# Kernel tuning notes

Measured on AMD Instinct MI355X. Metric: run time of the kernel, lower is better.

Reference implementation:

```python
import jax, jax.numpy as jnp
import numpy as np

B, H, W, C, HEADS, SR = 4, 64, 64, 256, 8, 2
D = C // HEADS            # head dim = 32
SCALE = D ** -0.5
EPS = 1e-6


def _conv(x, w, stride, pad, groups):
    return jax.lax.conv_general_dilated(
        x, w, (stride, stride), [(pad, pad), (pad, pad)],
        feature_group_count=groups,
        dimension_numbers=('NCHW', 'OIHW', 'NCHW'))


def setup_inputs() -> dict:
    key = jax.random.key(0)
    ks = jax.random.split(key, 9)
    s = lambda fan: 1.0 / np.sqrt(fan)
    return {
        'x': jax.random.normal(ks[0], (B, H * W, C), jnp.float32),
        'dw_w': jax.random.normal(ks[1], (C, 1, 3, 3), jnp.float32) * s(9),
        'dw_b': jnp.zeros((C,), jnp.float32),
        'pw_w': jax.random.normal(ks[2], (C, C, 1, 1), jnp.float32) * s(C),
        'pw_b': jnp.zeros((C,), jnp.float32),
        'sr_w': jax.random.normal(ks[3], (C, 1, 3, 3), jnp.float32) * s(9),
        'ln_g': jnp.ones((C,), jnp.float32),
        'ln_b': jnp.zeros((C,), jnp.float32),
        'kv_w': jax.random.normal(ks[4], (2 * C, C), jnp.float32) * s(C),
        'kv_b': jnp.zeros((2 * C,), jnp.float32),
        'proj_w': jax.random.normal(ks[5], (C, C), jnp.float32) * s(C),
        'proj_b': jnp.zeros((C,), jnp.float32),
    }


def reference(x, dw_w, dw_b, pw_w, pw_b, sr_w, ln_g, ln_b, kv_w, kv_b, proj_w, proj_b):
    Bx, N, Cx = x.shape
    # Q path: depthwise-separable conv on the spatial layout
    xq = x.reshape(Bx, H, W, Cx).transpose(0, 3, 1, 2)          # (B,C,H,W)
    q = _conv(xq, dw_w, 1, 1, Cx) + dw_b[None, :, None, None]    # depthwise 3x3
    q = _conv(q, pw_w, 1, 0, 1) + pw_b[None, :, None, None]      # pointwise 1x1
    # 'b (h d) l w -> b h (l w) d'
    q = q.reshape(Bx, HEADS, D, H * W).transpose(0, 1, 3, 2)     # (B,h,N,d)

    # SR path for K/V: strided depthwise conv + LayerNorm
    x_ = _conv(xq, sr_w, SR, SR // 2, Cx)                        # (B,C,H/SR,W/SR)
    x_ = x_.reshape(Bx, Cx, -1).transpose(0, 2, 1)               # (B,M,C)
    mu = jnp.mean(x_, axis=-1, keepdims=True)
    var = jnp.mean(jnp.square(x_ - mu), axis=-1, keepdims=True)
    x_ = (x_ - mu) * jax.lax.rsqrt(var + EPS) * ln_g + ln_b

    kv = x_ @ kv_w.T + kv_b                                      # (B,M,2C)
    M = kv.shape[1]
    kv = kv.reshape(Bx, M, 2, HEADS, D).transpose(2, 0, 3, 1, 4) # (2,B,h,M,d)
    k, v = kv[0], kv[1]

    attn = jnp.einsum('bhnd,bhmd->bhnm', q, k) * SCALE           # (B,h,N,M)
    attn = jax.nn.softmax(attn, axis=-1)
    out = jnp.einsum('bhnm,bhmd->bhnd', attn, v)                 # (B,h,N,d)
    out = out.transpose(0, 2, 1, 3).reshape(Bx, N, Cx)           # (B,N,C)
    return out @ proj_w.T + proj_b
```

## Files before the change

### kernel.cpp

```cpp
#include <hip/hip_runtime.h>
#include <math.h>

#define BB 4
#define HH 64
#define WW 64
#define CC 256
#define NN 4096
#define MM 1024
#define LN_EPS 1e-6f
#define SLF (0.17677669529663687f * 1.4426950408889634f)

typedef __attribute__((ext_vector_type(8)))  short short8;
typedef __attribute__((ext_vector_type(16))) float f32x16;
typedef __attribute__((ext_vector_type(4)))  unsigned int uint32x4;

__device__ __forceinline__ ushort f2bf(float f) {
  unsigned u = __builtin_bit_cast(unsigned, f);
  u += 0x7fffu + ((u >> 16) & 1u);
  return (ushort)(u >> 16);
}
__device__ __forceinline__ float bf2f(ushort h) {
  unsigned u = ((unsigned)h) << 16;
  return __builtin_bit_cast(float, u);
}
#if __has_builtin(__builtin_amdgcn_exp2f)
#define EXP2F(x) __builtin_amdgcn_exp2f(x)
#else
#define EXP2F(x) exp2f(x)
#endif

__global__ __launch_bounds__(256) void pre_fused(
    const float* __restrict__ x, const float* __restrict__ dw_w,
    const float* __restrict__ dw_b, const float* __restrict__ sr_w,
    const float* __restrict__ ln_g, const float* __restrict__ ln_b,
    const float* __restrict__ pw_w, const float* __restrict__ kv_w,
    const float* __restrict__ proj_w,
    ushort* __restrict__ q1b, ushort* __restrict__ xsr,
    ushort* __restrict__ pwB, ushort* __restrict__ kvB,
    ushort* __restrict__ pjH, ushort* __restrict__ pjL) {
  int bid = blockIdx.x;
  int c = threadIdx.x;
  if (bid < 4096) {
    int b = bid >> 10, m = bid & 1023;
    int my = m >> 5, mx = m & 31;
    const float* xb = x + (size_t)b * NN * CC + c;
    float acc = 0.f;
#pragma unroll
    for (int dy = 0; dy < 3; ++dy) {
      int iy = 2 * my + dy - 1;
      if (iy < 0 || iy >= HH) continue;
#pragma unroll
      for (int dx = 0; dx < 3; ++dx) {
        int ix = 2 * mx + dx - 1;
        if (ix < 0 || ix >= WW) continue;
        acc += xb[(size_t)(iy * WW + ix) * CC] * sr_w[c * 9 + dy * 3 + dx];
      }
    }
    float v1 = acc, v2 = acc * acc;
#pragma unroll
    for (int s = 1; s < 64; s <<= 1) {
      v1 += __shfl_xor(v1, s);
      v2 += __shfl_xor(v2, s);
    }
    __shared__ float r1[4], r2[4];
    int lane = c & 63, wv = c >> 6;
    if (lane == 0) { r1[wv] = v1; r2[wv] = v2; }
    __syncthreads();
    float s1 = r1[0] + r1[1] + r1[2] + r1[3];
    float s2 = r2[0] + r2[1] + r2[2] + r2[3];
    float mu = s1 * (1.f / 256.f);
    float var = s2 * (1.f / 256.f) - mu * mu;
    float yv = (acc - mu) * rsqrtf(var + LN_EPS) * ln_g[c] + ln_b[c];
    xsr[((size_t)b * MM + m) * CC + c] = f2bf(yv);
  } else if (bid < 6144) {
    int id = bid - 4096;
    int b = id >> 9, r = id & 511;
    int y = r >> 3, seg = r & 7;
    int x0 = seg * 8;
    float wr[9];
#pragma unroll
    for (int i = 0; i < 9; ++i) wr[i] = dw_w[c * 9 + i];
    float bi = dw_b[c];
    const float* xb = x + (size_t)b * NN * CC + c;
    bool okT = (y > 0), okB = (y < 63);
    float a0, a1, a2, b0, b1, b2;
    if (x0 == 0) {
      a0 = a1 = a2 = 0.f;
    } else {
      a0 = okT ? xb[(size_t)((y - 1) * 64 + x0 - 1) * CC] : 0.f;
      a1 = xb[(size_t)(y * 64 + x0 - 1) * CC];
      a2 = okB ? xb[(size_t)((y + 1) * 64 + x0 - 1) * CC] : 0.f;
    }
    b0 = okT ? xb[(size_t)((y - 1) * 64 + x0) * CC] : 0.f;
    b1 = xb[(size_t)(y * 64 + x0) * CC];
    b2 = okB ? xb[(size_t)((y + 1) * 64 + x0) * CC] : 0.f;
    ushort* ob = q1b + ((size_t)b * NN + y * 64) * CC + c;
#pragma unroll 8
    for (int xx = x0; xx < x0 + 8; ++xx) {
      float c0v, c1v, c2v;
      if (xx < 63) {
        c0v = okT ? xb[(size_t)((y - 1) * 64 + xx + 1) * CC] : 0.f;
        c1v = xb[(size_t)(y * 64 + xx + 1) * CC];
        c2v = okB ? xb[(size_t)((y + 1) * 64 + xx + 1) * CC] : 0.f;
      } else {
        c0v = c1v = c2v = 0.f;
      }
      float acc = bi;
      acc += a0 * wr[0] + b0 * wr[1] + c0v * wr[2];
      acc += a1 * wr[3] + b1 * wr[4] + c1v * wr[5];
      acc += a2 * wr[6] + b2 * wr[7] + c2v * wr[8];
      ob[(size_t)xx * CC] = f2bf(acc);
      a0 = b0; a1 = b1; a2 = b2;
      b0 = c0v; b1 = c1v; b2 = c2v;
    }
  } else if (bid < 6208) {
    int i0 = (bid - 6144) * 1024 + c * 4;
    float4 v = *(const float4*)&pw_w[i0];
    ushort tmp[4] = {f2bf(v.x), f2bf(v.y), f2bf(v.z), f2bf(v.w)};
    *(uint2*)&pwB[i0] = *(uint2*)tmp;
  } else if (bid < 6336) {
    int i0 = (bid - 6208) * 1024 + c * 4;
    float4 v = *(const float4*)&kv_w[i0];
    ushort tmp[4] = {f2bf(v.x), f2bf(v.y), f2bf(v.z), f2bf(v.w)};
    *(uint2*)&kvB[i0] = *(uint2*)tmp;
  } else {
    int i0 = (bid - 6336) * 1024 + c * 4;
    float4 v = *(const float4*)&proj_w[i0];
    float vv[4] = {v.x, v.y, v.z, v.w};
    ushort th[4], tl[4];
#pragma unroll
    for (int j = 0; j < 4; ++j) {
      th[j] = f2bf(vv[j]);
      tl[j] = f2bf(vv[j] - bf2f(th[j]));
    }
    *(uint2*)&pjH[i0] = *(uint2*)th;
    *(uint2*)&pjL[i0] = *(uint2*)tl;
  }
}

__global__ __launch_bounds__(256) void gemm_qkv(
    const ushort* __restrict__ q1b, const ushort* __restrict__ xsr,
    const ushort* __restrict__ pwB, const float* __restrict__ pw_b,
    const ushort* __restrict__ kvB, const float* __restrict__ kv_b,
    ushort* __restrict__ qB, ushort* __restrict__ kB,
    ushort* __restrict__ vT) {
  __shared__ ushort smem[2][128 * 40];
  int bid = blockIdx.x;
  bool is0 = bid < 1024;
  const ushort* A;
  const ushort* W;
  const float* bias;
  int r0, c0;
  if (is0) {
    A = q1b; W = pwB; bias = pw_b;
    r0 = (bid >> 2) * 64; c0 = (bid & 3) * 64;
  } else {
    int sid = bid - 1024;
    A = xsr; W = kvB; bias = kv_b;
    r0 = (sid >> 3) * 64; c0 = (sid & 7) * 64;
  }
  const bool vmode = (!is0) && (c0 >= 256);

  int t = threadIdx.x;
  int lane = t & 63, w = t >> 6;
  int l31 = lane & 31, half = lane >> 5;
  int wr = w >> 1, wc = w & 1;
  int rowA = t >> 2, kq = (t & 3) * 8;

  f32x16 acc;
#pragma unroll
  for (int i = 0; i < 16; ++i) acc[i] = 0.f;

  short8 ra[2], rw[2];
  auto prefetch = [&](int kc, int s) {
    ra[s] = *(const short8*)&A[(size_t)(r0 + rowA) * 256 + kc + kq];
    rw[s] = *(const short8*)&W[(size_t)(c0 + rowA) * 256 + kc + kq];
  };
  auto store = [&](ushort* buf, int s) {
    *(short8*)&buf[rowA * 40 + kq] = ra[s];
    *(short8*)&buf[64 * 40 + rowA * 40 + kq] = rw[s];
  };

  prefetch(0, 0);
  store(smem[0], 0);
  prefetch(32, 1);
  __syncthreads();
#pragma unroll
  for (int i = 0; i < 8; ++i) {
    ushort* cur = smem[i & 1];
    ushort* nxt = smem[(i & 1) ^ 1];
    if (i < 7) store(nxt, (i + 1) & 1);
    if (i < 6) prefetch((i + 2) * 32, i & 1);
#pragma unroll
    for (int ks = 0; ks < 2; ++ks) {
      short8 af = *(const short8*)&cur[(wr * 32 + l31) * 40 + ks * 16 + half * 8];
      short8 wf = *(const short8*)&cur[64 * 40 + (wc * 32 + l31) * 40 + ks * 16 + half * 8];
      if (vmode)
        acc = __builtin_amdgcn_mfma_f32_32x32x16_bf16(wf, af, acc, 0, 0, 0);
      else
        acc = __builtin_amdgcn_mfma_f32_32x32x16_bf16(af, wf, acc, 0, 0, 0);
    }
    __syncthreads();
  }

#pragma unroll
  for (int i = 0; i < 16; ++i) {
    int rl = (i & 3) + 8 * (i >> 2) + 4 * half;
    if (is0) {
      int r = r0 + wr * 32 + rl;
      int c = c0 + wc * 32 + l31;
      int b = r >> 12, n = r & 4095;
      int h = c >> 5, d = c & 31;
      qB[((size_t)(b * 8 + h) * NN + n) * 32 + d] =
          f2bf((acc[i] + bias[c]) * SLF);
    } else if (!vmode) {
      int r = r0 + wr * 32 + rl;
      int c = c0 + wc * 32 + l31;
      int b = r >> 10, m = r & 1023;
      int h = c >> 5, d = c & 31;
      kB[((size_t)(b * 8 + h) * MM + m) * 32 + d] = f2bf(acc[i] + bias[c]);
    } else {
      int c = c0 + wc * 32 + rl;
      int r = r0 + wr * 32 + l31;
      int b = r >> 10, m = r & 1023;
      int cv = c - 256;
      int h = cv >> 5, d = cv & 31;
      vT[((size_t)(b * 8 + h) * 32 + d) * MM + m] = f2bf(acc[i] + bias[c]);
    }
  }
}

__global__ __launch_bounds__(256, 4) void attn_mfma(
    const ushort* __restrict__ qB, const ushort* __restrict__ kB,
    const ushort* __restrict__ vT, ushort* __restrict__ aH,
    ushort* __restrict__ aL) {
  __shared__ ushort sKa[2][8][264];
  __shared__ ushort sVa[2][8][264];
  int t = threadIdx.x;
  int lane = t & 63, w = t >> 6;
  int l31 = lane & 31, half = lane >> 5;
  int bh = blockIdx.x;
  int b = bh >> 3, h = bh & 7;
  int q0 = blockIdx.y * 128;

  const ushort* qrow = qB + ((size_t)bh * NN + q0 + w * 32 + l31) * 32;
  short8 bq0 = *(const short8*)(qrow + half * 8);
  short8 bq1 = *(const short8*)(qrow + 16 + half * 8);

  const ushort* kbase = kB + (size_t)bh * MM * 32;
  const ushort* vbase = vT + (size_t)bh * 32 * MM;
  int krow = t >> 2, kq = (t & 3) * 8;
  int vd = t >> 3, vmo = (t & 7) * 8;
  int kreg_idx = (krow >> 5) * 4 + (kq >> 4) * 2 + ((kq >> 3) & 1);
  int klane = (krow & 31) * 8;
  int vreg_idx = (vmo >> 4) * 2 + ((vmo >> 3) & 1);
  int vlane = vd * 8;

  short8 kr[2], vr[2];
  kr[0] = *(const short8*)&kbase[(size_t)krow * 32 + kq];
  vr[0] = *(const short8*)&vbase[(size_t)vd * MM + vmo];
  kr[1] = *(const short8*)&kbase[(size_t)(64 + krow) * 32 + kq];
  vr[1] = *(const short8*)&vbase[(size_t)vd * MM + 64 + vmo];
  *(short8*)&sKa[0][kreg_idx][klane] = kr[0];
  *(short8*)&sVa[0][vreg_idx][vlane] = vr[0];

  f32x16 o;
#pragma unroll
  for (int i = 0; i < 16; ++i) o[i] = 0.f;
  float psum = 0.f;
  __syncthreads();

#pragma unroll 2
  for (int mc = 0; mc < 16; ++mc) {
    int cur = mc & 1, nxt = cur ^ 1;

    f32x16 st[2];
    __builtin_amdgcn_s_setprio(1);
#pragma unroll
    for (int tt = 0; tt < 2; ++tt) {
      short8 a0 = *(const short8*)&sKa[cur][tt * 4 + 0 + half][l31 * 8];
      short8 a1 = *(const short8*)&sKa[cur][tt * 4 + 2 + half][l31 * 8];
      f32x16 z;
#pragma unroll
      for (int i = 0; i < 16; ++i) z[i] = 0.f;
      z = __builtin_amdgcn_mfma_f32_32x32x16_bf16(a0, bq0, z, 0, 0, 0);
      z = __builtin_amdgcn_mfma_f32_32x32x16_bf16(a1, bq1, z, 0, 0, 0);
      st[tt] = z;
    }
    __builtin_amdgcn_s_setprio(0);

    if (mc < 15) {
      *(short8*)&sKa[nxt][kreg_idx][klane] = kr[nxt];
      *(short8*)&sVa[nxt][vreg_idx][vlane] = vr[nxt];
    }
    if (mc < 14) {
      int m2 = (mc + 2) * 64;
      kr[cur] = *(const short8*)&kbase[(size_t)(m2 + krow) * 32 + kq];
      vr[cur] = *(const short8*)&vbase[(size_t)vd * MM + m2 + vmo];
    }

    short8 bp[4];
#pragma unroll
    for (int tt = 0; tt < 2; ++tt) {
      float e[16];
#pragma unroll
      for (int i = 0; i < 16; ++i) e[i] = EXP2F(st[tt][i]);
#pragma unroll
      for (int i = 0; i < 16; i += 4)
        psum += (e[i] + e[i + 1]) + (e[i + 2] + e[i + 3]);
      unsigned pk[8];
#pragma unroll
      for (int j = 0; j < 8; ++j)
        asm("v_cvt_pk_bf16_f32 %0, %1, %2"
            : "=v"(pk[j]) : "v"(e[2 * j]), "v"(e[2 * j + 1]));
#pragma unroll
      for (int kbl = 0; kbl < 2; ++kbl) {
        unsigned w0 = pk[4 * kbl + 0], w2 = pk[4 * kbl + 2];
        unsigned w1 = pk[4 * kbl + 1], w3 = pk[4 * kbl + 3];
        asm("v_permlane32_swap_b32 %0, %1" : "+v"(w0), "+v"(w2));
        asm("v_permlane32_swap_b32 %0, %1" : "+v"(w1), "+v"(w3));
        uint32x4 wbits = {w0, w1, w2, w3};
        bp[2 * tt + kbl] = __builtin_bit_cast(short8, wbits);
      }
    }

    __builtin_amdgcn_s_setprio(1);
#pragma unroll
    for (int kb = 0; kb < 4; ++kb) {
      short8 av = *(const short8*)&sVa[cur][kb * 2 + half][l31 * 8];
      o = __builtin_amdgcn_mfma_f32_32x32x16_bf16(av, bp[kb], o, 0, 0, 0);
    }
    __builtin_amdgcn_s_setprio(0);

    __syncthreads();
  }

  float denom = psum + __shfl_xor(psum, 32);
  float inv = 1.f / denom;
  size_t rbase = ((size_t)b * NN + q0 + w * 32 + l31) * 256 + h * 32;
#pragma unroll
  for (int rg = 0; rg < 4; ++rg) {
#pragma unroll
    for (int j = 0; j < 4; ++j) {
      float v = o[rg * 4 + j] * inv;
      ushort hi = f2bf(v);
      ushort lo = f2bf(v - bf2f(hi));
      int d = rg * 8 + half * 4 + j;
      aH[rbase + d] = hi;
      aL[rbase + d] = lo;
    }
  }
}

__global__ __launch_bounds__(256) void gemm_proj(
    const ushort* __restrict__ A, const ushort* __restrict__ A2,
    const ushort* __restrict__ Whi, const ushort* __restrict__ Wlo,
    const float* __restrict__ bias, float* __restrict__ out) {
  __shared__ ushort smem[2][4 * 64 * 40];
  constexpr int OA = 0, OA2 = 64 * 40, OW = 2 * 64 * 40, OW2 = 3 * 64 * 40;
  int bid = blockIdx.x;
  int r0 = (bid >> 2) * 64, c0 = (bid & 3) * 64;

  int t = threadIdx.x;
  int lane = t & 63, w = t >> 6;
  int l31 = lane & 31, half = lane >> 5;
  int wr = w >> 1, wc = w & 1;
  int rowA = t >> 2, kq = (t & 3) * 8;

  f32x16 acc;
#pragma unroll
  for (int i = 0; i < 16; ++i) acc[i] = 0.f;

  short8 ra[2], ra2[2], rwh[2], rwl[2];
  auto prefetch = [&](int kc, int s) {
    ra[s]  = *(const short8*)&A[(size_t)(r0 + rowA) * 256 + kc + kq];
    ra2[s] = *(const short8*)&A2[(size_t)(r0 + rowA) * 256 + kc + kq];
    rwh[s] = *(const short8*)&Whi[(size_t)(c0 + rowA) * 256 + kc + kq];
    rwl[s] = *(const short8*)&Wlo[(size_t)(c0 + rowA) * 256 + kc + kq];
  };
  auto store = [&](ushort* buf, int s) {
    *(short8*)&buf[OA + rowA * 40 + kq] = ra[s];
    *(short8*)&buf[OA2 + rowA * 40 + kq] = ra2[s];
    *(short8*)&buf[OW + rowA * 40 + kq] = rwh[s];
    *(short8*)&buf[OW2 + rowA * 40 + kq] = rwl[s];
  };

  prefetch(0, 0);
  store(smem[0], 0);
  prefetch(32, 1);
  __syncthreads();
#pragma unroll
  for (int i = 0; i < 8; ++i) {
    ushort* cur = smem[i & 1];
    ushort* nxt = smem[(i & 1) ^ 1];
    if (i < 7) store(nxt, (i + 1) & 1);
    if (i < 6) prefetch((i + 2) * 32, i & 1);
#pragma unroll
    for (int ks = 0; ks < 2; ++ks) {
      int ro = (wr * 32 + l31) * 40 + ks * 16 + half * 8;
      int co = (wc * 32 + l31) * 40 + ks * 16 + half * 8;
      short8 af = *(const short8*)&cur[OA + ro];
      short8 af2 = *(const short8*)&cur[OA2 + ro];
      short8 wf = *(const short8*)&cur[OW + co];
      short8 wf2 = *(const short8*)&cur[OW2 + co];
      acc = __builtin_amdgcn_mfma_f32_32x32x16_bf16(af, wf, acc, 0, 0, 0);
      acc = __builtin_amdgcn_mfma_f32_32x32x16_bf16(af2, wf, acc, 0, 0, 0);
      acc = __builtin_amdgcn_mfma_f32_32x32x16_bf16(af, wf2, acc, 0, 0, 0);
    }
    __syncthreads();
  }

#pragma unroll
  for (int i = 0; i < 16; ++i) {
    int rl = (i & 3) + 8 * (i >> 2) + 4 * half;
    int r = r0 + wr * 32 + rl;
    int c = c0 + wc * 32 + l31;
    out[(size_t)r * 256 + c] = acc[i] + bias[c];
  }
}

extern "C" void kernel_launch(void* const* d_in, const int* in_sizes, int n_in,
                              void* d_out, int out_size, void* d_ws, size_t ws_size,
                              hipStream_t stream) {
  const float* x      = (const float*)d_in[0];
  const float* dw_w   = (const float*)d_in[1];
  const float* dw_b   = (const float*)d_in[2];
  const float* pw_w   = (const float*)d_in[3];
  const float* pw_b   = (const float*)d_in[4];
  const float* sr_w   = (const float*)d_in[5];
  const float* ln_g   = (const float*)d_in[6];
  const float* ln_b   = (const float*)d_in[7];
  const float* kv_w   = (const float*)d_in[8];
  const float* kv_b   = (const float*)d_in[9];
  const float* proj_w = (const float*)d_in[10];
  const float* proj_b = (const float*)d_in[11];
  float* out = (float*)d_out;

  char* ws = (char*)d_ws;
  ushort* q1b = (ushort*)(ws);
  ushort* xsr = (ushort*)(ws + (8u << 20));
  ushort* qB  = (ushort*)(ws + (16u << 20));
  ushort* kBp = (ushort*)(ws + (24u << 20));
  ushort* vTp = (ushort*)(ws + (26u << 20));
  ushort* aH  = (ushort*)(ws + (28u << 20));
  ushort* aL  = (ushort*)(ws + (36u << 20));
  ushort* pwB = (ushort*)(ws + (44u << 20));
  ushort* kvB = (ushort*)(ws + (44u << 20) + (512u << 10));
  ushort* pjH = (ushort*)(ws + (45u << 20));
  ushort* pjL = (ushort*)(ws + (45u << 20) + (512u << 10));

  pre_fused<<<dim3(6400), 256, 0, stream>>>(x, dw_w, dw_b, sr_w, ln_g, ln_b,
                                            pw_w, kv_w, proj_w,
                                            q1b, xsr, pwB, kvB, pjH, pjL);
  gemm_qkv<<<dim3(1536), 256, 0, stream>>>(q1b, xsr, pwB, pw_b, kvB, kv_b,
                                           qB, kBp, vTp);
  attn_mfma<<<dim3(32, 32), 256, 0, stream>>>(qB, kBp, vTp, aH, aL);
  gemm_proj<<<dim3(1024), 256, 0, stream>>>(aH, aL, pjH, pjL, proj_b, out);
}
```

Measured before the change: 155.1 us.

## Vectorize pre-pass per wave and double query rows per attention block

```diff
diff --git a/kernel.cpp b/kernel.cpp
--- a/kernel.cpp
+++ b/kernel.cpp
@@ -39,12 +39,19 @@
     ushort* __restrict__ pwB, ushort* __restrict__ kvB,
     ushort* __restrict__ pjH, ushort* __restrict__ pjL) {
   int bid = blockIdx.x;
-  int c = threadIdx.x;
-  if (bid < 4096) {
-    int b = bid >> 10, m = bid & 1023;
+  int t = threadIdx.x;
+  int wv = t >> 6, lane = t & 63;
+  if (bid < 1024) {
+    int g = bid * 4 + wv;
+    int b = g >> 10, m = g & 1023;
     int my = m >> 5, mx = m & 31;
-    const float* xb = x + (size_t)b * NN * CC + c;
-    float acc = 0.f;
+    int c4 = lane * 4;
+    float wl[36];
+#pragma unroll
+    for (int k = 0; k < 9; ++k)
+      *(float4*)&wl[4 * k] = *(const float4*)&sr_w[c4 * 9 + 4 * k];
+    const float* xb = x + (size_t)b * NN * CC + c4;
+    float4 acc = {0.f, 0.f, 0.f, 0.f};
 #pragma unroll
     for (int dy = 0; dy < 3; ++dy) {
       int iy = 2 * my + dy - 1;
@@ -53,78 +60,100 @@
       for (int dx = 0; dx < 3; ++dx) {
         int ix = 2 * mx + dx - 1;
         if (ix < 0 || ix >= WW) continue;
-        acc += xb[(size_t)(iy * WW + ix) * CC] * sr_w[c * 9 + dy * 3 + dx];
+        float4 xv = *(const float4*)&xb[(size_t)(iy * WW + ix) * CC];
+        int tap = dy * 3 + dx;
+        acc.x += xv.x * wl[0 + tap];
+        acc.y += xv.y * wl[9 + tap];
+        acc.z += xv.z * wl[18 + tap];
+        acc.w += xv.w * wl[27 + tap];
       }
     }
-    float v1 = acc, v2 = acc * acc;
+    float v1 = (acc.x + acc.y) + (acc.z + acc.w);
+    float v2 = (acc.x * acc.x + acc.y * acc.y) + (acc.z * acc.z + acc.w * acc.w);
 #pragma unroll
     for (int s = 1; s < 64; s <<= 1) {
       v1 += __shfl_xor(v1, s);
       v2 += __shfl_xor(v2, s);
     }
-    __shared__ float r1[4], r2[4];
-    int lane = c & 63, wv = c >> 6;
-    if (lane == 0) { r1[wv] = v1; r2[wv] = v2; }
-    __syncthreads();
-    float s1 = r1[0] + r1[1] + r1[2] + r1[3];
-    float s2 = r2[0] + r2[1] + r2[2] + r2[3];
-    float mu = s1 * (1.f / 256.f);
-    float var = s2 * (1.f / 256.f) - mu * mu;
-    float yv = (acc - mu) * rsqrtf(var + LN_EPS) * ln_g[c] + ln_b[c];
-    xsr[((size_t)b * MM + m) * CC + c] = f2bf(yv);
-  } else if (bid < 6144) {
-    int id = bid - 4096;
-    int b = id >> 9, r = id & 511;
+    float mu = v1 * (1.f / 256.f);
+    float var = v2 * (1.f / 256.f) - mu * mu;
+    float rs = rsqrtf(var + LN_EPS);
+    float4 g4 = *(const float4*)&ln_g[c4];
+    float4 b4 = *(const float4*)&ln_b[c4];
+    ushort o4[4];
+    o4[0] = f2bf((acc.x - mu) * rs * g4.x + b4.x);
+    o4[1] = f2bf((acc.y - mu) * rs * g4.y + b4.y);
+    o4[2] = f2bf((acc.z - mu) * rs * g4.z + b4.z);
+    o4[3] = f2bf((acc.w - mu) * rs * g4.w + b4.w);
+    *(uint2*)&xsr[((size_t)b * MM + m) * CC + c4] = *(uint2*)o4;
+  } else if (bid < 1536) {
+    int R = (bid - 1024) * 4 + wv;
+    int b = R >> 9, r = R & 511;
     int y = r >> 3, seg = r & 7;
     int x0 = seg * 8;
-    float wr[9];
-#pragma unroll
-    for (int i = 0; i < 9; ++i) wr[i] = dw_w[c * 9 + i];
-    float bi = dw_b[c];
-    const float* xb = x + (size_t)b * NN * CC + c;
+    int c4 = lane * 4;
+    float wl[36];
+#pragma unroll
+    for (int k = 0; k < 9; ++k)
+      *(float4*)&wl[4 * k] = *(const float4*)&dw_w[c4 * 9 + 4 * k];
+    float4 bi = *(const float4*)&dw_b[c4];
+    const float* xb = x + (size_t)b * NN * CC + c4;
     bool okT = (y > 0), okB = (y < 63);
-    float a0, a1, a2, b0, b1, b2;
+    const float4 z4 = {0.f, 0.f, 0.f, 0.f};
+#define LD4(pt) (*(const float4*)&xb[(size_t)(pt) * CC])
+    float4 a0, a1, a2, b0, b1, b2;
     if (x0 == 0) {
-      a0 = a1 = a2 = 0.f;
+      a0 = a1 = a2 = z4;
     } else {
-      a0 = okT ? xb[(size_t)((y - 1) * 64 + x0 - 1) * CC] : 0.f;
-      a1 = xb[(size_t)(y * 64 + x0 - 1) * CC];
-      a2 = okB ? xb[(size_t)((y + 1) * 64 + x0 - 1) * CC] : 0.f;
-    }
-    b0 = okT ? xb[(size_t)((y - 1) * 64 + x0) * CC] : 0.f;
-    b1 = xb[(size_t)(y * 64 + x0) * CC];
-    b2 = okB ? xb[(size_t)((y + 1) * 64 + x0) * CC] : 0.f;
-    ushort* ob = q1b + ((size_t)b * NN + y * 64) * CC + c;
+      a0 = okT ? LD4((y - 1) * 64 + x0 - 1) : z4;
+      a1 = LD4(y * 64 + x0 - 1);
+      a2 = okB ? LD4((y + 1) * 64 + x0 - 1) : z4;
+    }
+    b0 = okT ? LD4((y - 1) * 64 + x0) : z4;
+    b1 = LD4(y * 64 + x0);
+    b2 = okB ? LD4((y + 1) * 64 + x0) : z4;
+    ushort* ob = q1b + ((size_t)b * NN + y * 64) * CC + c4;
 #pragma unroll 8
     for (int xx = x0; xx < x0 + 8; ++xx) {
-      float c0v, c1v, c2v;
+      float4 c0v, c1v, c2v;
       if (xx < 63) {
-        c0v = okT ? xb[(size_t)((y - 1) * 64 + xx + 1) * CC] : 0.f;
-        c1v = xb[(size_t)(y * 64 + xx + 1) * CC];
-        c2v = okB ? xb[(size_t)((y + 1) * 64 + xx + 1) * CC] : 0.f;
+        c0v = okT ? LD4((y - 1) * 64 + xx + 1) : z4;
+        c1v = LD4(y * 64 + xx + 1);
+        c2v = okB ? LD4((y + 1) * 64 + xx + 1) : z4;
       } else {
-        c0v = c1v = c2v = 0.f;
+        c0v = c1v = c2v = z4;
       }
-      float acc = bi;
-      acc += a0 * wr[0] + b0 * wr[1] + c0v * wr[2];
-      acc += a1 * wr[3] + b1 * wr[4] + c1v * wr[5];
-      acc += a2 * wr[6] + b2 * wr[7] + c2v * wr[8];
-      ob[(size_t)xx * CC] = f2bf(acc);
+      float4 acc = bi;
+      acc.x += a0.x * wl[0] + b0.x * wl[1] + c0v.x * wl[2] +
+               a1.x * wl[3] + b1.x * wl[4] + c1v.x * wl[5] +
+               a2.x * wl[6] + b2.x * wl[7] + c2v.x * wl[8];
+      acc.y += a0.y * wl[9] + b0.y * wl[10] + c0v.y * wl[11] +
+               a1.y * wl[12] + b1.y * wl[13] + c1v.y * wl[14] +
+               a2.y * wl[15] + b2.y * wl[16] + c2v.y * wl[17];
+      acc.z += a0.z * wl[18] + b0.z * wl[19] + c0v.z * wl[20] +
+               a1.z * wl[21] + b1.z * wl[22] + c1v.z * wl[23] +
+               a2.z * wl[24] + b2.z * wl[25] + c2v.z * wl[26];
+      acc.w += a0.w * wl[27] + b0.w * wl[28] + c0v.w * wl[29] +
+               a1.w * wl[30] + b1.w * wl[31] + c1v.w * wl[32] +
+               a2.w * wl[33] + b2.w * wl[34] + c2v.w * wl[35];
+      ushort o4[4] = {f2bf(acc.x), f2bf(acc.y), f2bf(acc.z), f2bf(acc.w)};
+      *(uint2*)&ob[(size_t)xx * CC] = *(uint2*)o4;
       a0 = b0; a1 = b1; a2 = b2;
       b0 = c0v; b1 = c1v; b2 = c2v;
     }
-  } else if (bid < 6208) {
-    int i0 = (bid - 6144) * 1024 + c * 4;
+#undef LD4
+  } else if (bid < 1600) {
+    int i0 = (bid - 1536) * 1024 + t * 4;
     float4 v = *(const float4*)&pw_w[i0];
     ushort tmp[4] = {f2bf(v.x), f2bf(v.y), f2bf(v.z), f2bf(v.w)};
     *(uint2*)&pwB[i0] = *(uint2*)tmp;
-  } else if (bid < 6336) {
-    int i0 = (bid - 6208) * 1024 + c * 4;
+  } else if (bid < 1728) {
+    int i0 = (bid - 1600) * 1024 + t * 4;
     float4 v = *(const float4*)&kv_w[i0];
     ushort tmp[4] = {f2bf(v.x), f2bf(v.y), f2bf(v.z), f2bf(v.w)};
     *(uint2*)&kvB[i0] = *(uint2*)tmp;
   } else {
-    int i0 = (bid - 6336) * 1024 + c * 4;
+    int i0 = (bid - 1728) * 1024 + t * 4;
     float4 v = *(const float4*)&proj_w[i0];
     float vv[4] = {v.x, v.y, v.z, v.w};
     ushort th[4], tl[4];
@@ -230,7 +259,7 @@
   }
 }
 
-__global__ __launch_bounds__(256, 4) void attn_mfma(
+__global__ __launch_bounds__(256, 2) void attn_mfma(
     const ushort* __restrict__ qB, const ushort* __restrict__ kB,
     const ushort* __restrict__ vT, ushort* __restrict__ aH,
     ushort* __restrict__ aL) {
@@ -241,11 +270,14 @@
   int l31 = lane & 31, half = lane >> 5;
   int bh = blockIdx.x;
   int b = bh >> 3, h = bh & 7;
-  int q0 = blockIdx.y * 128;
+  int q0 = blockIdx.y * 256;
 
   const ushort* qrow = qB + ((size_t)bh * NN + q0 + w * 32 + l31) * 32;
-  short8 bq0 = *(const short8*)(qrow + half * 8);
-  short8 bq1 = *(const short8*)(qrow + 16 + half * 8);
+  short8 bqa0 = *(const short8*)(qrow + half * 8);
+  short8 bqa1 = *(const short8*)(qrow + 16 + half * 8);
+  const ushort* qrow2 = qrow + 128 * 32;
+  short8 bqb0 = *(const short8*)(qrow2 + half * 8);
+  short8 bqb1 = *(const short8*)(qrow2 + 16 + half * 8);
 
   const ushort* kbase = kB + (size_t)bh * MM * 32;
   const ushort* vbase = vT + (size_t)bh * 32 * MM;
@@ -264,16 +296,13 @@
   *(short8*)&sKa[0][kreg_idx][klane] = kr[0];
   *(short8*)&sVa[0][vreg_idx][vlane] = vr[0];
 
-  f32x16 o;
-#pragma unroll
-  for (int i = 0; i < 16; ++i) o[i] = 0.f;
-  float psum = 0.f;
+  f32x16 oa, ob_;
+#pragma unroll
+  for (int i = 0; i < 16; ++i) { oa[i] = 0.f; ob_[i] = 0.f; }
+  float psa = 0.f, psb = 0.f;
   __syncthreads();
 
-#pragma unroll 2
-  for (int mc = 0; mc < 16; ++mc) {
-    int cur = mc & 1, nxt = cur ^ 1;
-
+  auto doset = [&](short8 q0f, short8 q1f, f32x16& o, float& psum, int cur) {
     f32x16 st[2];
     __builtin_amdgcn_s_setprio(1);
 #pragma unroll
@@ -283,21 +312,11 @@
       f32x16 z;
 #pragma unroll
       for (int i = 0; i < 16; ++i) z[i] = 0.f;
-      z = __builtin_amdgcn_mfma_f32_32x32x16_bf16(a0, bq0, z, 0, 0, 0);
-      z = __builtin_amdgcn_mfma_f32_32x32x16_bf16(a1, bq1, z, 0, 0, 0);
+      z = __builtin_amdgcn_mfma_f32_32x32x16_bf16(a0, q0f, z, 0, 0, 0);
+      z = __builtin_amdgcn_mfma_f32_32x32x16_bf16(a1, q1f, z, 0, 0, 0);
       st[tt] = z;
     }
     __builtin_amdgcn_s_setprio(0);
-
-    if (mc < 15) {
-      *(short8*)&sKa[nxt][kreg_idx][klane] = kr[nxt];
-      *(short8*)&sVa[nxt][vreg_idx][vlane] = vr[nxt];
-    }
-    if (mc < 14) {
-      int m2 = (mc + 2) * 64;
-      kr[cur] = *(const short8*)&kbase[(size_t)(m2 + krow) * 32 + kq];
-      vr[cur] = *(const short8*)&vbase[(size_t)vd * MM + m2 + vmo];
-    }
 
     short8 bp[4];
 #pragma unroll
@@ -331,23 +350,61 @@
       o = __builtin_amdgcn_mfma_f32_32x32x16_bf16(av, bp[kb], o, 0, 0, 0);
     }
     __builtin_amdgcn_s_setprio(0);
+  };
+
+#pragma unroll 2
+  for (int mc = 0; mc < 16; ++mc) {
+    int cur = mc & 1, nxt = cur ^ 1;
+
+    doset(bqa0, bqa1, oa, psa, cur);
+
+    if (mc < 15) {
+      *(short8*)&sKa[nxt][kreg_idx][klane] = kr[nxt];
+      *(short8*)&sVa[nxt][vreg_idx][vlane] = vr[nxt];
+    }
+    if (mc < 14) {
+      int m2 = (mc + 2) * 64;
+      kr[cur] = *(const short8*)&kbase[(size_t)(m2 + krow) * 32 + kq];
+      vr[cur] = *(const short8*)&vbase[(size_t)vd * MM + m2 + vmo];
+    }
+
+    doset(bqb0, bqb1, ob_, psb, cur);
 
     __syncthreads();
   }
 
-  float denom = psum + __shfl_xor(psum, 32);
-  float inv = 1.f / denom;
-  size_t rbase = ((size_t)b * NN + q0 + w * 32 + l31) * 256 + h * 32;
-#pragma unroll
-  for (int rg = 0; rg < 4; ++rg) {
-#pragma unroll
-    for (int j = 0; j < 4; ++j) {
-      float v = o[rg * 4 + j] * inv;
-      ushort hi = f2bf(v);
-      ushort lo = f2bf(v - bf2f(hi));
-      int d = rg * 8 + half * 4 + j;
-      aH[rbase + d] = hi;
-      aL[rbase + d] = lo;
+  {
+    float denom = psa + __shfl_xor(psa, 32);
+    float inv = 1.f / denom;
+    size_t rbase = ((size_t)b * NN + q0 + w * 32 + l31) * 256 + h * 32;
+#pragma unroll
+    for (int rg = 0; rg < 4; ++rg) {
+#pragma unroll
+      for (int j = 0; j < 4; ++j) {
+        float v = oa[rg * 4 + j] * inv;
+        ushort hi = f2bf(v);
+        ushort lo = f2bf(v - bf2f(hi));
+        int d = rg * 8 + half * 4 + j;
+        aH[rbase + d] = hi;
+        aL[rbase + d] = lo;
+      }
+    }
+  }
+  {
+    float denom = psb + __shfl_xor(psb, 32);
+    float inv = 1.f / denom;
+    size_t rbase = ((size_t)b * NN + q0 + 128 + w * 32 + l31) * 256 + h * 32;
+#pragma unroll
+    for (int rg = 0; rg < 4; ++rg) {
+#pragma unroll
+      for (int j = 0; j < 4; ++j) {
+        float v = ob_[rg * 4 + j] * inv;
+        ushort hi = f2bf(v);
+        ushort lo = f2bf(v - bf2f(hi));
+        int d = rg * 8 + half * 4 + j;
+        aH[rbase + d] = hi;
+        aL[rbase + d] = lo;
+      }
     }
   }
 }
@@ -449,11 +506,11 @@
   ushort* pjH = (ushort*)(ws + (45u << 20));
   ushort* pjL = (ushort*)(ws + (45u << 20) + (512u << 10));
 
-  pre_fused<<<dim3(6400), 256, 0, stream>>>(x, dw_w, dw_b, sr_w, ln_g, ln_b,
+  pre_fused<<<dim3(1792), 256, 0, stream>>>(x, dw_w, dw_b, sr_w, ln_g, ln_b,
                                             pw_w, kv_w, proj_w,
                                             q1b, xsr, pwB, kvB, pjH, pjL);
   gemm_qkv<<<dim3(1536), 256, 0, stream>>>(q1b, xsr, pwB, pw_b, kvB, kv_b,
                                            qB, kBp, vTp);
-  attn_mfma<<<dim3(32, 32), 256, 0, stream>>>(qB, kBp, vTp, aH, aL);
+  attn_mfma<<<dim3(32, 16), 256, 0, stream>>>(qB, kBp, vTp, aH, aL);
   gemm_proj<<<dim3(1024), 256, 0, stream>>>(aH, aL, pjH, pjL, proj_b, out);
 }
```

New measurement: 165.1 us. +6.5%, slower.
